# Kernel optimization log

Measured on AMD Instinct MI355X. Metric: run time of the kernel, lower is better.

The kernel has to match this reference:

```python
import jax, jax.numpy as jnp
import numpy as np

HEADS = 8
DIM_HEAD = 64
MP_ADD_T = 0.3
EPS = 1e-4


def normalize_weight(w, eps=EPS):
    # Karras forced weight norm: per-output-channel L2 norm over all other dims
    dims = tuple(range(1, w.ndim))
    n = jnp.sqrt(jnp.sum(w * w, axis=dims, keepdims=True))
    alpha = np.sqrt(n.size / w.size)  # = 1/sqrt(fan_in)
    return w / (eps + alpha * n)


def pixel_norm(t, eps=EPS):
    # F.normalize(dim=-1) * sqrt(d): x / max(||x||, eps) * sqrt(d)
    n = jnp.sqrt(jnp.sum(t * t, axis=-1, keepdims=True))
    return t / jnp.maximum(n, eps) * np.sqrt(t.shape[-1])


def conv1x1(x, w):
    # x: [b,c,h,w], w: [o,c] (normalized weight / sqrt(fan_in))
    wn = normalize_weight(w) / np.sqrt(w.shape[1])  # fan_in = dim_in * 1 * 1
    return jnp.einsum('bchw,oc->bohw', x, wn)


def setup_inputs() -> dict:
    key = jax.random.key(0)
    k1, k2, k3, k4 = jax.random.split(key, 4)
    b, c, h, w = 16, 512, 32, 32
    hidden = HEADS * DIM_HEAD
    return {
        'x': jax.random.normal(k1, (b, c, h, w), dtype=jnp.float32),
        'w_qkv': jax.random.normal(k2, (hidden * 3, c), dtype=jnp.float32),
        'w_out': jax.random.normal(k3, (c, hidden), dtype=jnp.float32),
        'mem_kv': jax.random.normal(k4, (2, HEADS, 4, DIM_HEAD), dtype=jnp.float32),
    }


def reference(x, w_qkv, w_out, mem_kv):
    b, c, h, w = x.shape
    n = h * w
    qkv = conv1x1(x, w_qkv)  # [b, 3*hidden, h, w]
    q, k, v = jnp.split(qkv, 3, axis=1)

    def to_heads(t):
        # b (h c) x y -> b h (x y) c
        return t.reshape(b, HEADS, DIM_HEAD, n).transpose(0, 1, 3, 2)

    q, k, v = map(to_heads, (q, k, v))
    mk = jnp.broadcast_to(mem_kv[0], (b,) + mem_kv[0].shape)  # [b,h,m,d]
    mv = jnp.broadcast_to(mem_kv[1], (b,) + mem_kv[1].shape)
    k = jnp.concatenate([mk, k], axis=2)
    v = jnp.concatenate([mv, v], axis=2)

    q, k, v = map(pixel_norm, (q, k, v))

    sim = jnp.einsum('bhid,bhjd->bhij', q, k) * (DIM_HEAD ** -0.5)
    attn = jax.nn.softmax(sim, axis=-1)  # dropout is identity in eval
    out = jnp.einsum('bhij,bhjd->bhid', attn, v)  # [b,h,n,d]

    # b h (x y) d -> b (h d) x y
    out = out.transpose(0, 1, 3, 2).reshape(b, HEADS * DIM_HEAD, h, w)
    out = conv1x1(out, w_out)

    # MPAdd: magnitude-preserving residual
    t = MP_ADD_T
    den = np.sqrt((1 - t) ** 2 + t ** 2)
    return (out * (1.0 - t) + x * t) / den
```

## Files before the change

kernel.cpp:

```cpp
#include <hip/hip_runtime.h>
#include <hip/hip_bf16.h>
#include <math.h>

#define HEADS 8
#define DIMH 64
#define NPIX 1024
#define BATCH 16
#define CIN 512
#define HIDDEN 512
#define OQKV 1536

typedef __attribute__((ext_vector_type(8))) short v8s;
typedef __attribute__((ext_vector_type(4))) float v4f;
typedef __attribute__((ext_vector_type(4))) int v4i;

#define MFMA16(a, b, c) __builtin_amdgcn_mfma_f32_16x16x32_bf16(a, b, c, 0, 0, 0)

__device__ inline unsigned pkbf(float lo, float hi) {
    unsigned r;
    asm("v_cvt_pk_bf16_f32 %0, %1, %2" : "=v"(r) : "v"(lo), "v"(hi));
    return r;
}
__device__ inline ushort bf16u(float f) {
    __hip_bfloat16 h = __float2bfloat16(f);
    return *(ushort*)&h;
}
__device__ inline float exp2i(float x) {
    float r;
    asm("v_exp_f32 %0, %1" : "=v"(r) : "v"(x));
    return r;
}
__device__ inline void gload16(const ushort* g, ushort* l) {
    __builtin_amdgcn_global_load_lds(
        (const __attribute__((address_space(1))) void*)g,
        (__attribute__((address_space(3))) void*)l, 16, 0, 0);
}

#define INVLN2 1.44269504088896f
#define BIAS2  12.2629078475662f

__global__ __launch_bounds__(256) void prep_fused(
    const float* __restrict__ x,
    const float* __restrict__ wq, const float* __restrict__ wo,
    const float* __restrict__ mem_kv,
    ushort* __restrict__ Xt, ushort* __restrict__ wn,
    __hip_bfloat16* __restrict__ mk, __hip_bfloat16* __restrict__ mv,
    float* __restrict__ msk)
{
    int bid = blockIdx.x;
    if (bid < 2048) {
        int b = bid >> 7, rem = bid & 127;
        int c0 = (rem >> 4) * 64, p0 = (rem & 15) * 64;
        __shared__ ushort lds[64][72];
        int tid = threadIdx.x;
        int cl = tid >> 2;
        int pl = (tid & 3) * 16;
        const float* src = x + ((size_t)b * CIN + c0 + cl) * NPIX + p0 + pl;
        #pragma unroll
        for (int j = 0; j < 4; j++) {
            float4 v = *(const float4*)(src + j * 4);
            lds[cl][pl + j * 4 + 0] = bf16u(v.x);
            lds[cl][pl + j * 4 + 1] = bf16u(v.y);
            lds[cl][pl + j * 4 + 2] = bf16u(v.z);
            lds[cl][pl + j * 4 + 3] = bf16u(v.w);
        }
        __syncthreads();
        int pw = tid >> 2;
        int cs = (tid & 3) * 16;
        union { ushort u[16]; uint4 q[2]; } tmp;
        #pragma unroll
        for (int j = 0; j < 16; j++) tmp.u[j] = lds[cs + j][pw];
        ushort* dst = Xt + ((size_t)b * NPIX + p0 + pw) * CIN + c0 + cs;
        *(uint4*)(dst) = tmp.q[0];
        *(uint4*)(dst + 8) = tmp.q[1];
    } else if (bid < 4096) {
        int row = bid - 2048;
        const float* src = (row < OQKV) ? (wq + (size_t)row * CIN)
                                        : (wo + (size_t)(row - OQKV) * CIN);
        int t = threadIdx.x;
        float v0 = src[t];
        float v1 = src[t + 256];
        float ss = v0 * v0 + v1 * v1;
        #pragma unroll
        for (int off = 32; off >= 1; off >>= 1) ss += __shfl_xor(ss, off);
        __shared__ float red[4];
        if ((t & 63) == 0) red[t >> 6] = ss;
        __syncthreads();
        float total = red[0] + red[1] + red[2] + red[3];
        const float RSQRT512 = 0.044194173824159216f;
        const float SQRT512  = 22.627416997969522f;
        float scale = 1.0f / ((1e-4f + sqrtf(total) * RSQRT512) * SQRT512);
        ushort* dst = wn + (size_t)row * CIN;
        dst[t] = bf16u(v0 * scale);
        dst[t + 256] = bf16u(v1 * scale);
    } else {
        if (threadIdx.x < 64) {
            int h = bid - 4096;
            int lane = threadIdx.x;
            #pragma unroll
            for (int m = 0; m < 4; m++) {
                float kvv = mem_kv[((size_t)h * 4 + m) * 64 + lane];
                float vvv = mem_kv[((size_t)(HEADS + h) * 4 + m) * 64 + lane];
                float ssk = kvv * kvv, ssv = vvv * vvv;
                #pragma unroll
                for (int off = 32; off >= 1; off >>= 1) {
                    ssk += __shfl_xor(ssk, off);
                    ssv += __shfl_xor(ssv, off);
                }
                float sck = 8.0f / fmaxf(sqrtf(ssk), 1e-4f);
                float scv = 8.0f / fmaxf(sqrtf(ssv), 1e-4f);
                mk[((size_t)h * 16 + m) * 64 + lane] = __float2bfloat16(kvv);
                mv[((size_t)h * 64 + lane) * 32 + m] = __float2bfloat16(vvv * scv);
                if (lane == 0) { msk[h * 16 + m] = sck; }
            }
            #pragma unroll
            for (int m = 4; m < 16; m++)
                mk[((size_t)h * 16 + m) * 64 + lane] = __float2bfloat16(0.f);
            #pragma unroll
            for (int m = 4; m < 32; m++)
                mv[((size_t)h * 64 + lane) * 32 + m] = __float2bfloat16(0.f);
            if (lane >= 4 && lane < 16) msk[h * 16 + lane] = 0.f;
        }
    }
}

__global__ __launch_bounds__(256) void gemm_qkv_mfma(
    const ushort* __restrict__ Wall,
    const ushort* __restrict__ Xt,
    ushort* __restrict__ Qb, ushort* __restrict__ Kb, ushort* __restrict__ Vb,
    float* __restrict__ qsA)
{
    int bid = blockIdx.x;
    int xcd = bid & 7;
    int rest = bid >> 3;
    int bh2 = rest / 96;
    int r = rest - bh2 * 96;
    int b = xcd + (bh2 << 3);
    int yy = r % 12;
    int pp = r / 12;

    int p0 = pp * 128;
    int isV = (yy >= 8) ? 1 : 0;
    int o0 = (isV ? (yy - 8) : yy) * 128;
    const ushort* Wsrc = Wall + (isV ? (size_t)1024 * CIN : 0);

    int tid = threadIdx.x;
    int wave = tid >> 6, lane = tid & 63;
    int wy = wave >> 1, wx = wave & 1;
    int col = lane & 15, lg = lane >> 4;
    int pw = p0 + wx * 64;
    int ow = o0 + wy * 64;

    __shared__ __align__(16) ushort sW[128 * 64];
    __shared__ __align__(16) ushort sX[128 * 64];

    int rIn = lane >> 3;
    int chS = (lane & 7) ^ rIn;
    int rowStage = wave * 32 + rIn;
    const ushort* gW = Wsrc + (size_t)(o0 + rowStage) * CIN + chS * 8;
    const ushort* gX = Xt + ((size_t)b * NPIX + p0 + rowStage) * CIN + chS * 8;

    v4f acc[4][4];
    #pragma unroll
    for (int i = 0; i < 4; i++)
        #pragma unroll
        for (int j = 0; j < 4; j++) acc[i][j] = (v4f){0.f, 0.f, 0.f, 0.f};

    const ushort* sA = isV ? sX : sW;
    const ushort* sB = isV ? sW : sX;
    int rowA = (isV ? wx : wy) * 64 + col;
    int rowB = (isV ? wy : wx) * 64 + col;
    int c7 = col & 7;

    #pragma unroll 1
    for (int c0 = 0; c0 < CIN; c0 += 64) {
        #pragma unroll
        for (int j = 0; j < 4; j++) {
            gload16(gW + (size_t)j * 8 * CIN + c0, &sW[(wave * 4 + j) * 512]);
            gload16(gX + (size_t)j * 8 * CIN + c0, &sX[(wave * 4 + j) * 512]);
        }
        __syncthreads();
        #pragma unroll
        for (int hh = 0; hh < 2; hh++) {
            int ch = (hh * 4 + lg) ^ c7;
            v8s af[4], bf[4];
            #pragma unroll
            for (int i = 0; i < 4; i++) {
                af[i] = *(const v8s*)&sA[(rowA + i * 16) * 64 + ch * 8];
                bf[i] = *(const v8s*)&sB[(rowB + i * 16) * 64 + ch * 8];
            }
            #pragma unroll
            for (int i = 0; i < 4; i++)
                #pragma unroll
                for (int j = 0; j < 4; j++)
                    acc[i][j] = MFMA16(af[i], bf[j], acc[i][j]);
        }
        __syncthreads();
    }

    if (!isV) {
        int part = ow >> 9;
        int h = (ow >> 6) & 7;
        int bh = b * HEADS + h;

        float ssq[4];
        #pragma unroll
        for (int pt = 0; pt < 4; pt++) {
            float s = 0.f;
            #pragma unroll
            for (int dt = 0; dt < 4; dt++)
                #pragma unroll
                for (int r2 = 0; r2 < 4; r2++) s += acc[dt][pt][r2] * acc[dt][pt][r2];
            s += __shfl_xor(s, 16);
            s += __shfl_xor(s, 32);
            ssq[pt] = s;
        }
        if (part == 0) {
            if (lg == 0) {
                #pragma unroll
                for (int pt = 0; pt < 4; pt++)
                    qsA[(size_t)bh * NPIX + pw + pt * 16 + col] =
                        1.0f / fmaxf(sqrtf(ssq[pt]), 1e-4f);
            }
            ushort* dst = Qb + (size_t)bh * NPIX * DIMH;
            #pragma unroll
            for (int pt = 0; pt < 4; pt++) {
                int p = pw + pt * 16 + col;
                #pragma unroll
                for (int dt = 0; dt < 4; dt++) {
                    uint2 uu;
                    uu.x = pkbf(acc[dt][pt][0], acc[dt][pt][1]);
                    uu.y = pkbf(acc[dt][pt][2], acc[dt][pt][3]);
                    *(uint2*)(dst + (size_t)p * DIMH + dt * 16 + 4 * lg) = uu;
                }
            }
        } else {
            float scl[4];
            #pragma unroll
            for (int pt = 0; pt < 4; pt++)
                scl[pt] = 8.0f / fmaxf(sqrtf(ssq[pt]), 1e-4f);
            ushort* dst = Kb + (size_t)bh * NPIX * DIMH;
            #pragma unroll
            for (int pt = 0; pt < 4; pt++) {
                int p = pw + pt * 16 + col;
                #pragma unroll
                for (int dt = 0; dt < 4; dt++) {
                    uint2 uu;
                    uu.x = pkbf(acc[dt][pt][0] * scl[pt], acc[dt][pt][1] * scl[pt]);
                    uu.y = pkbf(acc[dt][pt][2] * scl[pt], acc[dt][pt][3] * scl[pt]);
                    *(uint2*)(dst + (size_t)p * DIMH + dt * 16 + 4 * lg) = uu;
                }
            }
        }
    } else {
        int h = (ow >> 6) & 7;
        int bh = b * HEADS + h;

        float scl[4][4];
        #pragma unroll
        for (int pt = 0; pt < 4; pt++) {
            #pragma unroll
            for (int r2 = 0; r2 < 4; r2++) {
                float s = acc[pt][0][r2] * acc[pt][0][r2] + acc[pt][1][r2] * acc[pt][1][r2]
                        + acc[pt][2][r2] * acc[pt][2][r2] + acc[pt][3][r2] * acc[pt][3][r2];
                s += __shfl_xor(s, 1);
                s += __shfl_xor(s, 2);
                s += __shfl_xor(s, 4);
                s += __shfl_xor(s, 8);
                scl[pt][r2] = 8.0f / fmaxf(sqrtf(s), 1e-4f);
            }
        }
        #pragma unroll
        for (int ot = 0; ot < 4; ot++) {
            int d = ot * 16 + col;
            #pragma unroll
            for (int pt = 0; pt < 4; pt++) {
                uint2 uu;
                uu.x = pkbf(acc[pt][ot][0] * scl[pt][0], acc[pt][ot][1] * scl[pt][1]);
                uu.y = pkbf(acc[pt][ot][2] * scl[pt][2], acc[pt][ot][3] * scl[pt][3]);
                *(uint2*)(Vb + ((size_t)bh * DIMH + d) * NPIX + pw + pt * 16 + 4 * lg) = uu;
            }
        }
    }
}

__global__ __launch_bounds__(256, 2) void attn_mfma_kernel(
    const __hip_bfloat16* __restrict__ Qb,
    const __hip_bfloat16* __restrict__ Kb,
    const __hip_bfloat16* __restrict__ Vb,
    const float* __restrict__ qsA,
    const __hip_bfloat16* __restrict__ mk, const __hip_bfloat16* __restrict__ mv,
    const float* __restrict__ msk,
    ushort* __restrict__ attT)
{
    int bid = blockIdx.x;
    int bh = bid & 127;
    int qb = bid >> 7;
    int b = bh >> 3, h = bh & 7;
    int wave = threadIdx.x >> 6, lane = threadIdx.x & 63;
    int col = lane & 15, lg = lane >> 4;
    int q0 = qb * 256 + wave * 64;

    const __hip_bfloat16* Qbase = Qb + ((size_t)bh * NPIX + q0) * DIMH;
    const __hip_bfloat16* Kbase = Kb + (size_t)bh * NPIX * DIMH;
    const __hip_bfloat16* Vbase = Vb + (size_t)bh * DIMH * NPIX;

    v8s qf[4][2];
    float myqs[4];
    #pragma unroll
    for (int qt = 0; qt < 4; qt++) {
        #pragma unroll
        for (int dh = 0; dh < 2; dh++)
            qf[qt][dh] = *(const v8s*)(Qbase + (qt * 16 + col) * DIMH + dh * 32 + 8 * lg);
        myqs[qt] = qsA[(size_t)bh * NPIX + q0 + qt * 16 + col] * INVLN2;
    }

    v4f o_[4][4];
    #pragma unroll
    for (int qt = 0; qt < 4; qt++)
        #pragma unroll
        for (int dt = 0; dt < 4; dt++) o_[qt][dt] = (v4f){0.f, 0.f, 0.f, 0.f};
    float l_[4] = {0.f, 0.f, 0.f, 0.f};

    int srcA = ((lg & 1) << 5) + col;
    int srcB = srcA + 16;
    bool hig = (lg >= 2);

    {
        const __hip_bfloat16* mkh = mk + (size_t)h * 16 * DIMH;
        v8s kf0 = *(const v8s*)(mkh + col * DIMH + 8 * lg);
        v8s kf1 = *(const v8s*)(mkh + col * DIMH + 32 + 8 * lg);
        v8s vfm[4];
        #pragma unroll
        for (int dt = 0; dt < 4; dt++)
            vfm[dt] = *(const v8s*)(mv + ((size_t)h * DIMH + dt * 16 + col) * 32 + 8 * lg);
        float4 ksm = *(const float4*)&msk[h * 16 + 4 * lg];
        float ksr[4] = {ksm.x, ksm.y, ksm.z, ksm.w};

        #pragma unroll
        for (int qt = 0; qt < 4; qt++) {
            v4f c0 = (v4f){0.f, 0.f, 0.f, 0.f};
            c0 = MFMA16(kf0, qf[qt][0], c0);
            c0 = MFMA16(kf1, qf[qt][1], c0);
            float p0[4];
            #pragma unroll
            for (int r = 0; r < 4; r++) {
                float t = __builtin_fmaf(c0[r], myqs[qt] * ksr[r], -BIAS2);
                p0[r] = (lg == 0) ? exp2i(t) : 0.f;
                l_[qt] += p0[r];
            }
            unsigned A0 = pkbf(p0[0], p0[1]);
            unsigned A1 = pkbf(p0[2], p0[3]);
            int a0 = __shfl((int)A0, srcA), a1 = __shfl((int)A1, srcA);
            int a2 = __shfl((int)A0, srcB), a3 = __shfl((int)A1, srcB);
            v4i w;
            w.x = hig ? 0 : a0; w.y = hig ? 0 : a1;
            w.z = hig ? 0 : a2; w.w = hig ? 0 : a3;
            v8s pf = __builtin_bit_cast(v8s, w);
            #pragma unroll
            for (int dt = 0; dt < 4; dt++)
                o_[qt][dt] = MFMA16(vfm[dt], pf, o_[qt][dt]);
        }
    }

    v8s kfA[4], vfA[4], kfB[4], vfB[4];

    #define LOADK(dst, kk) { \
        const __hip_bfloat16* Kr = Kbase + (size_t)(kk) * DIMH; \
        dst[0] = *(const v8s*)(Kr + col * DIMH + 8 * lg); \
        dst[1] = *(const v8s*)(Kr + col * DIMH + 32 + 8 * lg); \
        dst[2] = *(const v8s*)(Kr + (16 + col) * DIMH + 8 * lg); \
        dst[3] = *(const v8s*)(Kr + (16 + col) * DIMH + 32 + 8 * lg); }
    #define LOADV(dst, kk) { \
        _Pragma("unroll") \
        for (int dt = 0; dt < 4; dt++) \
            dst[dt] = *(const v8s*)(Vbase + (size_t)(dt * 16 + col) * NPIX + (kk) + 8 * lg); }

    #define COMPUTE(kf, vf, kk) { \
        _Pragma("unroll") \
        for (int qt = 0; qt < 4; qt++) { \
            v4f c0 = (v4f){0.f, 0.f, 0.f, 0.f}; \
            v4f c1 = (v4f){0.f, 0.f, 0.f, 0.f}; \
            __builtin_amdgcn_s_setprio(1); \
            c0 = MFMA16(kf[0], qf[qt][0], c0); \
            c0 = MFMA16(kf[1], qf[qt][1], c0); \
            c1 = MFMA16(kf[2], qf[qt][0], c1); \
            c1 = MFMA16(kf[3], qf[qt][1], c1); \
            __builtin_amdgcn_s_setprio(0); \
            float p0[4], p1[4]; \
            _Pragma("unroll") \
            for (int r = 0; r < 4; r++) { \
                p0[r] = exp2i(__builtin_fmaf(c0[r], myqs[qt], -BIAS2)); \
                p1[r] = exp2i(__builtin_fmaf(c1[r], myqs[qt], -BIAS2)); \
                l_[qt] += p0[r] + p1[r]; \
            } \
            unsigned A0 = pkbf(p0[0], p0[1]); \
            unsigned A1 = pkbf(p0[2], p0[3]); \
            unsigned B0 = pkbf(p1[0], p1[1]); \
            unsigned B1 = pkbf(p1[2], p1[3]); \
            int a0 = __shfl((int)A0, srcA), a1 = __shfl((int)A1, srcA); \
            int a2 = __shfl((int)A0, srcB), a3 = __shfl((int)A1, srcB); \
            int b0 = __shfl((int)B0, srcA), b1 = __shfl((int)B1, srcA); \
            int b2 = __shfl((int)B0, srcB), b3 = __shfl((int)B1, srcB); \
            v4i w; \
            w.x = hig ? b0 : a0; w.y = hig ? b1 : a1; \
            w.z = hig ? b2 : a2; w.w = hig ? b3 : a3; \
            v8s pf = __builtin_bit_cast(v8s, w); \
            __builtin_amdgcn_s_setprio(1); \
            _Pragma("unroll") \
            for (int dt = 0; dt < 4; dt++) \
                o_[qt][dt] = MFMA16(vf[dt], pf, o_[qt][dt]); \
            __builtin_amdgcn_s_setprio(0); \
        } }

    LOADK(kfA, 0);
    LOADV(vfA, 0);
    #pragma unroll 1
    for (int k0 = 0; k0 < NPIX; k0 += 64) {
        LOADK(kfB, k0 + 32);
        LOADV(vfB, k0 + 32);
        COMPUTE(kfA, vfA, k0);
        LOADK(kfA, k0 + 64);
        LOADV(vfA, k0 + 64);
        COMPUTE(kfB, vfB, k0 + 32);
    }

    #pragma unroll
    for (int qt = 0; qt < 4; qt++) {
        float l = l_[qt];
        l += __shfl_xor(l, 16);
        l += __shfl_xor(l, 32);
        float invl = 1.0f / l;
        ushort* at = attT + ((size_t)(b * NPIX + q0 + qt * 16 + col)) * HIDDEN + h * DIMH;
        #pragma unroll
        for (int dt = 0; dt < 4; dt++) {
            uint2 uu;
            uu.x = pkbf(o_[qt][dt][0] * invl, o_[qt][dt][1] * invl);
            uu.y = pkbf(o_[qt][dt][2] * invl, o_[qt][dt][3] * invl);
            *(uint2*)(at + dt * 16 + 4 * lg) = uu;
        }
    }
    #undef LOADK
    #undef LOADV
    #undef COMPUTE
}

__global__ __launch_bounds__(256) void gemm_out_mfma(
    const ushort* __restrict__ Wo,
    const ushort* __restrict__ attT,
    const float* __restrict__ x, float* __restrict__ out)
{
    int b = blockIdx.z;
    int o0 = blockIdx.y * 128;
    int p0 = blockIdx.x * 128;
    int tid = threadIdx.x;
    int wave = tid >> 6, lane = tid & 63;
    int wy = wave >> 1, wx = wave & 1;
    int col = lane & 15, lg = lane >> 4;
    int ow = o0 + wy * 64, pw = p0 + wx * 64;

    __shared__ __align__(16) ushort sAa[128 * 64];
    __shared__ __align__(16) ushort sBb[128 * 64];

    int rIn = lane >> 3;
    int chS = (lane & 7) ^ rIn;
    int rowStage = wave * 32 + rIn;
    const ushort* gA = attT + ((size_t)b * NPIX + p0 + rowStage) * HIDDEN + chS * 8;
    const ushort* gB = Wo + (size_t)(o0 + rowStage) * HIDDEN + chS * 8;

    v4f acc[4][4];
    #pragma unroll
    for (int i = 0; i < 4; i++)
        #pragma unroll
        for (int j = 0; j < 4; j++) acc[i][j] = (v4f){0.f, 0.f, 0.f, 0.f};

    int rowA = wx * 64 + col;
    int rowB = wy * 64 + col;
    int c7 = col & 7;

    #pragma unroll 1
    for (int c0 = 0; c0 < HIDDEN; c0 += 64) {
        #pragma unroll
        for (int j = 0; j < 4; j++) {
            gload16(gA + (size_t)j * 8 * HIDDEN + c0, &sAa[(wave * 4 + j) * 512]);
            gload16(gB + (size_t)j * 8 * HIDDEN + c0, &sBb[(wave * 4 + j) * 512]);
        }
        __syncthreads();
        #pragma unroll
        for (int hh = 0; hh < 2; hh++) {
            int ch = (hh * 4 + lg) ^ c7;
            v8s af[4], bf[4];
            #pragma unroll
            for (int i = 0; i < 4; i++) {
                af[i] = *(const v8s*)&sAa[(rowA + i * 16) * 64 + ch * 8];
                bf[i] = *(const v8s*)&sBb[(rowB + i * 16) * 64 + ch * 8];
            }
            #pragma unroll
            for (int i = 0; i < 4; i++)
                #pragma unroll
                for (int j = 0; j < 4; j++)
                    acc[i][j] = MFMA16(af[i], bf[j], acc[i][j]);
        }
        __syncthreads();
    }

    const float INV_DEN = 1.3130643285972254f;
    #pragma unroll
    for (int pt = 0; pt < 4; pt++) {
        #pragma unroll
        for (int ot = 0; ot < 4; ot++) {
            size_t base = ((size_t)b * HIDDEN + ow + ot * 16 + col) * NPIX
                        + pw + pt * 16 + 4 * lg;
            float4 res = *(const float4*)&x[base];
            float4 y;
            y.x = (acc[pt][ot][0] * 0.7f + res.x * 0.3f) * INV_DEN;
            y.y = (acc[pt][ot][1] * 0.7f + res.y * 0.3f) * INV_DEN;
            y.z = (acc[pt][ot][2] * 0.7f + res.z * 0.3f) * INV_DEN;
            y.w = (acc[pt][ot][3] * 0.7f + res.w * 0.3f) * INV_DEN;
            *(float4*)&out[base] = y;
        }
    }
}

extern "C" void kernel_launch(void* const* d_in, const int* in_sizes, int n_in,
                              void* d_out, int out_size, void* d_ws, size_t ws_size,
                              hipStream_t stream)
{
    const float* x      = (const float*)d_in[0];
    const float* w_qkv  = (const float*)d_in[1];
    const float* w_out  = (const float*)d_in[2];
    const float* mem_kv = (const float*)d_in[3];
    float* out = (float*)d_out;

    char* ws = (char*)d_ws;
    ushort* wnB = (ushort*)ws; ws += (size_t)2048 * CIN * 2;
    ushort* Xt  = (ushort*)ws; ws += (size_t)BATCH * NPIX * CIN * 2;
    ushort* Qb  = (ushort*)ws; ws += (size_t)BATCH * HEADS * NPIX * DIMH * 2;
    ushort* Kb  = (ushort*)ws; ws += (size_t)BATCH * HEADS * NPIX * DIMH * 2;
    ushort* Vb  = (ushort*)ws; ws += (size_t)BATCH * HEADS * NPIX * DIMH * 2;
    ushort* attT = (ushort*)ws; ws += (size_t)BATCH * NPIX * HIDDEN * 2;
    float* qsA = (float*)ws;  ws += (size_t)BATCH * HEADS * NPIX * 4;
    float* msk = (float*)ws;  ws += 8 * 16 * 4;
    __hip_bfloat16* mk = (__hip_bfloat16*)ws; ws += (size_t)8 * 16 * 64 * 2;
    __hip_bfloat16* mv = (__hip_bfloat16*)ws; ws += (size_t)8 * 64 * 32 * 2;

    prep_fused<<<4104, 256, 0, stream>>>(
        x, w_qkv, w_out, mem_kv, Xt, wnB, mk, mv, msk);

    gemm_qkv_mfma<<<1536, 256, 0, stream>>>(
        wnB, Xt, Qb, Kb, Vb, qsA);

    attn_mfma_kernel<<<512, 256, 0, stream>>>(
        (const __hip_bfloat16*)Qb, (const __hip_bfloat16*)Kb,
        (const __hip_bfloat16*)Vb, qsA, mk, mv, msk, attT);

    gemm_out_mfma<<<dim3(8, 4, BATCH), 256, 0, stream>>>(
        wnB + (size_t)OQKV * CIN, attT, x, out);
}
```

Before: 155.4 us.

## Stage K/V tiles in swizzled LDS shared across waves with double buffering

Before this change, each of the four waves loaded its own copy of the K and V fragments straight from global memory. Now the block cooperatively copies 64-key K/V tiles into double-buffered, XOR-swizzled shared memory using gload16 direct-to-LDS loads, and all waves read their fragments from there. This cuts global/L2 traffic by sharing K/V across the four waves and uses the swizzle to avoid LDS bank conflicts. The cost is a block-wide barrier per tile and 32KB of LDS, which may limit occupancy under launch_bounds(256,2).

```diff
diff --git a/kernel.cpp b/kernel.cpp
--- a/kernel.cpp
+++ b/kernel.cpp
@@ -301,9 +301,15 @@
     int col = lane & 15, lg = lane >> 4;
     int q0 = qb * 256 + wave * 64;
 
+    __shared__ __align__(16) ushort sK[2][64 * 64];
+    __shared__ __align__(16) ushort sV[2][64 * 64];
+
+    const ushort* Kg = (const ushort*)Kb + (size_t)bh * NPIX * DIMH;
+    const ushort* Vg = (const ushort*)Vb + (size_t)bh * DIMH * NPIX;
     const __hip_bfloat16* Qbase = Qb + ((size_t)bh * NPIX + q0) * DIMH;
-    const __hip_bfloat16* Kbase = Kb + (size_t)bh * NPIX * DIMH;
-    const __hip_bfloat16* Vbase = Vb + (size_t)bh * DIMH * NPIX;
+
+    int rIn = lane >> 3;
+    int chS = (lane & 7) ^ rIn;
 
     v8s qf[4][2];
     float myqs[4];
@@ -363,20 +369,26 @@
         }
     }
 
-    v8s kfA[4], vfA[4], kfB[4], vfB[4];
-
-    #define LOADK(dst, kk) { \
-        const __hip_bfloat16* Kr = Kbase + (size_t)(kk) * DIMH; \
-        dst[0] = *(const v8s*)(Kr + col * DIMH + 8 * lg); \
-        dst[1] = *(const v8s*)(Kr + col * DIMH + 32 + 8 * lg); \
-        dst[2] = *(const v8s*)(Kr + (16 + col) * DIMH + 8 * lg); \
-        dst[3] = *(const v8s*)(Kr + (16 + col) * DIMH + 32 + 8 * lg); }
-    #define LOADV(dst, kk) { \
+    #define STAGE(cur, kk) { \
+        _Pragma("unroll") \
+        for (int j = 0; j < 2; j++) { \
+            gload16(Kg + ((size_t)(kk) + wave * 16 + j * 8 + rIn) * 64 + chS * 8, \
+                    &sK[cur][wave * 1024 + j * 512]); \
+            gload16(Vg + ((size_t)(wave * 16 + j * 8 + rIn)) * 1024 + (kk) + chS * 8, \
+                    &sV[cur][wave * 1024 + j * 512]); \
+        } }
+
+    #define COMPUTE_LDS(cur, ks) { \
+        v8s kf[4], vf[4]; \
+        int rk0 = (ks) * 32 + col, rk1 = rk0 + 16; \
+        int sw = col & 7; \
+        kf[0] = *(const v8s*)&sK[cur][rk0 * 64 + ((lg    ) ^ sw) * 8]; \
+        kf[1] = *(const v8s*)&sK[cur][rk0 * 64 + ((lg + 4) ^ sw) * 8]; \
+        kf[2] = *(const v8s*)&sK[cur][rk1 * 64 + ((lg    ) ^ sw) * 8]; \
+        kf[3] = *(const v8s*)&sK[cur][rk1 * 64 + ((lg + 4) ^ sw) * 8]; \
         _Pragma("unroll") \
         for (int dt = 0; dt < 4; dt++) \
-            dst[dt] = *(const v8s*)(Vbase + (size_t)(dt * 16 + col) * NPIX + (kk) + 8 * lg); }
-
-    #define COMPUTE(kf, vf, kk) { \
+            vf[dt] = *(const v8s*)&sV[cur][(dt * 16 + col) * 64 + (((ks) * 4 + lg) ^ sw) * 8]; \
         _Pragma("unroll") \
         for (int qt = 0; qt < 4; qt++) { \
             v4f c0 = (v4f){0.f, 0.f, 0.f, 0.f}; \
@@ -413,16 +425,16 @@
             __builtin_amdgcn_s_setprio(0); \
         } }
 
-    LOADK(kfA, 0);
-    LOADV(vfA, 0);
+    int cur = 0;
+    STAGE(0, 0);
+    __syncthreads();
     #pragma unroll 1
-    for (int k0 = 0; k0 < NPIX; k0 += 64) {
-        LOADK(kfB, k0 + 32);
-        LOADV(vfB, k0 + 32);
-        COMPUTE(kfA, vfA, k0);
-        LOADK(kfA, k0 + 64);
-        LOADV(vfA, k0 + 64);
-        COMPUTE(kfB, vfB, k0 + 32);
+    for (int t = 0; t < 16; t++) {
+        if (t < 15) STAGE(cur ^ 1, (t + 1) * 64);
+        COMPUTE_LDS(cur, 0);
+        COMPUTE_LDS(cur, 1);
+        __syncthreads();
+        cur ^= 1;
     }
 
     #pragma unroll
@@ -440,9 +452,8 @@
             *(uint2*)(at + dt * 16 + 4 * lg) = uu;
         }
     }
-    #undef LOADK
-    #undef LOADV
-    #undef COMPUTE
+    #undef STAGE
+    #undef COMPUTE_LDS
 }
 
 __global__ __launch_bounds__(256) void gemm_out_mfma(
```

Result: faster. 141.7 us (median of 3 runs) (-8.8%).
